# Performance work log

Hardware: AMD Instinct MI355X
Metric: run time of the kernel (lower is better)

The kernel has to match this reference:

```python
import jax, jax.numpy as jnp
import numpy as np

N = 1024
INTER_CH = 10      # C(4,2) + (8-4)
HIDDEN_CH = 32
OUT_CH = 1
THRESH = 4
TOP_K = 8
INTERACT = 4


def setup_inputs() -> dict:
    key = jax.random.key(0)
    k1, k2, k3, k4, k5 = jax.random.split(key, 5)
    x = jax.random.normal(k1, (16, N, N), dtype=jnp.float32)
    is_active_flags = jnp.ones((16,), dtype=bool)
    # 1x1 conv params (stored as dense matrices; kernel_size=1)
    w1 = jax.random.normal(k2, (HIDDEN_CH, INTER_CH), dtype=jnp.float32) / np.sqrt(INTER_CH)
    b1 = jax.random.normal(k3, (HIDDEN_CH, 1, 1), dtype=jnp.float32) * 0.01
    w2 = jax.random.normal(k4, (OUT_CH, HIDDEN_CH), dtype=jnp.float32) / np.sqrt(HIDDEN_CH)
    b2 = jax.random.normal(k5, (OUT_CH, 1, 1), dtype=jnp.float32) * 0.01
    return {"x": x, "is_active_flags": is_active_flags, "w1": w1, "b1": b1, "w2": w2, "b2": b2}


def reference(x, is_active_flags, w1, b1, w2, b2):
    gate_active = jnp.sum(is_active_flags) >= THRESH

    def _active_path(operand):
        inputs, mask = operand                       # (16, n, n), (16,)
        _, slogdet = jnp.linalg.slogdet(inputs)      # (16,)
        scores = jnp.where(mask, slogdet, -jnp.inf)
        _, indices = jax.lax.top_k(scores, TOP_K)
        top_x = inputs[indices]                      # (8, n, n)
        top_interact_x = top_x[:INTERACT]            # (4, n, n)
        next_preserve_x = top_x[INTERACT:]           # (4, n, n)
        idx1, idx2 = jnp.triu_indices(INTERACT, k=1)  # 6 pairs
        pairs = jnp.matmul(top_interact_x[idx1], top_interact_x[idx2])  # (6, n, n)
        concat = jnp.concatenate([pairs, next_preserve_x], axis=0)      # (10, n, n)
        hidden = jnp.einsum('oc,chw->ohw', w1, concat) + b1             # 1x1 conv
        out = jnp.einsum('oc,chw->ohw', w2, hidden) + b2                # 1x1 conv
        return (out, jnp.array(True))

    def _inactive_path(operand):
        inputs, _ = operand
        _, n, m = inputs.shape
        return (jnp.zeros((OUT_CH, n, m), dtype=jnp.float32), jnp.array(False))

    out, out_active = jax.lax.cond(gate_active, _active_path, _inactive_path, (x, is_active_flags))
    return (out, out_active)
```

## Files before the change

### kernel.cpp

```cpp
#include <hip/hip_runtime.h>
#include <math.h>

#define N 1024
#define NN (N*N)

__global__ void init_kernel(double* scores) {
  int t = threadIdx.x;
  if (t < 16) scores[t] = 0.0;
}

__global__ __launch_bounds__(256) void copy_kernel(const float4* __restrict__ src,
                                                   float4* __restrict__ dst) {
  int i = blockIdx.x * 256 + threadIdx.x;
  dst[i] = src[i];
}

__global__ __launch_bounds__(256, 1) void panel_kernel(float* __restrict__ lu,
                                                       unsigned short* __restrict__ rowsrc,
                                                       double* __restrict__ scores,
                                                       int c0) {
  __shared__ __align__(16) float prow[32];
  __shared__ float ujjS[32];
  __shared__ float redv[2][4];
  __shared__ int   redk[2][4];
  __shared__ int Vv[1024];
  __shared__ int Pv[1024];
  const int m = blockIdx.x;
  float* A = lu + (size_t)m * NN;
  const int R = N - c0;
  const int tid = threadIdx.x;

  const float4 z4 = make_float4(0.f, 0.f, 0.f, 0.f);
  float4 r0_0=z4, r0_1=z4, r0_2=z4, r0_3=z4, r0_4=z4, r0_5=z4, r0_6=z4, r0_7=z4;
  float4 r1_0=z4, r1_1=z4, r1_2=z4, r1_3=z4, r1_4=z4, r1_5=z4, r1_6=z4, r1_7=z4;
  float4 r2_0=z4, r2_1=z4, r2_2=z4, r2_3=z4, r2_4=z4, r2_5=z4, r2_6=z4, r2_7=z4;
  float4 r3_0=z4, r3_1=z4, r3_2=z4, r3_3=z4, r3_4=z4, r3_5=z4, r3_6=z4, r3_7=z4;

  const bool ld0 = (tid           < R);
  const bool ld1 = (tid + 256     < R);
  const bool ld2 = (tid + 512     < R);
  const bool ld3 = (tid + 768     < R);
  bool act0 = ld0, act1 = ld1, act2 = ld2, act3 = ld3;

#define LOADK(K) \
  if (ld##K) { \
    const float* src_ = A + (size_t)(c0 + tid + (K << 8)) * N + c0; \
    r##K##_0 = *(const float4*)(src_ +  0); \
    r##K##_1 = *(const float4*)(src_ +  4); \
    r##K##_2 = *(const float4*)(src_ +  8); \
    r##K##_3 = *(const float4*)(src_ + 12); \
    r##K##_4 = *(const float4*)(src_ + 16); \
    r##K##_5 = *(const float4*)(src_ + 20); \
    r##K##_6 = *(const float4*)(src_ + 24); \
    r##K##_7 = *(const float4*)(src_ + 28); \
  }
  LOADK(0) LOADK(1) LOADK(2) LOADK(3)
#undef LOADK

  for (int i = tid; i < R; i += 256) { Vv[i] = i; Pv[i] = i; }

  {
    float bval = -1.0f; int brow = 0x7fffffff;
    if (act0) { float v = fabsf(r0_0.x); if (v > bval || (v == bval && tid       < brow)) { bval = v; brow = tid;       } }
    if (act1) { float v = fabsf(r1_0.x); if (v > bval || (v == bval && tid + 256 < brow)) { bval = v; brow = tid + 256; } }
    if (act2) { float v = fabsf(r2_0.x); if (v > bval || (v == bval && tid + 512 < brow)) { bval = v; brow = tid + 512; } }
    if (act3) { float v = fabsf(r3_0.x); if (v > bval || (v == bval && tid + 768 < brow)) { bval = v; brow = tid + 768; } }
    #pragma unroll
    for (int mask = 32; mask; mask >>= 1) {
      float ov = __shfl_xor(bval, mask);
      int   orr = __shfl_xor(brow, mask);
      if (ov > bval || (ov == bval && orr < brow)) { bval = ov; brow = orr; }
    }
    if ((tid & 63) == 0) { redv[0][tid >> 6] = bval; redk[0][tid >> 6] = brow; }
  }
  __syncthreads();

  #pragma unroll 1
  for (int j = 0; j < 32; ++j) {
    int pcur;
    {
      const int pb = j & 1;
      float bv = redv[pb][0]; int bk = redk[pb][0];
      float v1 = redv[pb][1]; int k1 = redk[pb][1];
      float v2 = redv[pb][2]; int k2 = redk[pb][2];
      float v3 = redv[pb][3]; int k3 = redk[pb][3];
      if (v1 > bv || (v1 == bv && k1 < bk)) { bv = v1; bk = k1; }
      if (v2 > bv || (v2 == bv && k2 < bk)) { bv = v2; bk = k2; }
      if (v3 > bv || (v3 == bv && k3 < bk)) { bv = v3; bk = k3; }
      pcur = bk;
    }
    if (tid == (pcur & 255)) {
      const int kk = pcur >> 8;
      float4* pd = (float4*)prow;
#define PUBQ(Q) { \
      float4 v = r0_##Q; \
      if (kk == 1) v = r1_##Q; \
      if (kk == 2) v = r2_##Q; \
      if (kk == 3) v = r3_##Q; \
      pd[Q] = v; }
      PUBQ(0) PUBQ(1) PUBQ(2) PUBQ(3) PUBQ(4) PUBQ(5) PUBQ(6) PUBQ(7)
#undef PUBQ
      if (kk == 0) act0 = false;
      else if (kk == 1) act1 = false;
      else if (kk == 2) act2 = false;
      else act3 = false;
    }
    if (tid == 0) {
      int b  = Pv[pcur];
      int pa = Vv[j];
      Vv[j] = pcur; Vv[b] = pa;
      Pv[pcur] = j; Pv[pa] = b;
    }
    __syncthreads();

    const float ujj = prow[j];
    if (tid == 0) ujjS[j] = ujj;
    const float rujj = 1.0f / ujj;
    const int qj = j >> 2, ej = j & 3;
    const int jn = j + 1;
    const int qn = (j < 31) ? (jn >> 2) : -1, en = jn & 3;

    float4 u4_0=z4, u4_1=z4, u4_2=z4, u4_3=z4, u4_4=z4, u4_5=z4, u4_6=z4, u4_7=z4;
#define UREAD(Q) if (4 * Q + 3 >= j) u4_##Q = *(const float4*)&prow[4 * Q];
    UREAD(0) UREAD(1) UREAD(2) UREAD(3) UREAD(4) UREAD(5) UREAD(6) UREAD(7)
#undef UREAD

    float bval = -1.0f; int brow = 0x7fffffff;
#define QSTEP(K,Q) \
    if (Q >= qj) { \
      float4 v = r##K##_##Q; \
      if (Q == qj) { \
        float aj = (ej == 0) ? v.x : (ej == 1) ? v.y : (ej == 2) ? v.z : v.w; \
        l = aj * rujj; \
        if (ej == 0)      { v.x = l; v.y -= l * u4_##Q.y; v.z -= l * u4_##Q.z; v.w -= l * u4_##Q.w; } \
        else if (ej == 1) { v.y = l; v.z -= l * u4_##Q.z; v.w -= l * u4_##Q.w; } \
        else if (ej == 2) { v.z = l; v.w -= l * u4_##Q.w; } \
        else              { v.w = l; } \
      } else { \
        v.x -= l * u4_##Q.x; v.y -= l * u4_##Q.y; v.z -= l * u4_##Q.z; v.w -= l * u4_##Q.w; \
      } \
      if (Q == qn) nv = (en == 0) ? v.x : (en == 1) ? v.y : (en == 2) ? v.z : v.w; \
      r##K##_##Q = v; \
    }
#define UPDK(K) \
    if (act##K) { \
      const int rr_ = tid + (K << 8); \
      float l = 0.0f, nv = 0.0f; \
      QSTEP(K,0) QSTEP(K,1) QSTEP(K,2) QSTEP(K,3) QSTEP(K,4) QSTEP(K,5) QSTEP(K,6) QSTEP(K,7) \
      if (j < 31) { \
        float av = fabsf(nv); \
        if (av > bval || (av == bval && rr_ < brow)) { bval = av; brow = rr_; } \
      } \
    }
    UPDK(0) UPDK(1) UPDK(2) UPDK(3)
#undef UPDK
#undef QSTEP

    if (j < 31) {
      #pragma unroll
      for (int mask = 32; mask; mask >>= 1) {
        float ov = __shfl_xor(bval, mask);
        int   orr = __shfl_xor(brow, mask);
        if (ov > bval || (ov == bval && orr < brow)) { bval = ov; brow = orr; }
      }
      if ((tid & 63) == 0) { redv[jn & 1][tid >> 6] = bval; redk[jn & 1][tid >> 6] = brow; }
    }
    __syncthreads();
  }

#define STOREK(K) \
  if (ld##K) { \
    float* dst_ = A + (size_t)(c0 + tid + (K << 8)) * N + c0; \
    *(float4*)(dst_ +  0) = r##K##_0; \
    *(float4*)(dst_ +  4) = r##K##_1; \
    *(float4*)(dst_ +  8) = r##K##_2; \
    *(float4*)(dst_ + 12) = r##K##_3; \
    *(float4*)(dst_ + 16) = r##K##_4; \
    *(float4*)(dst_ + 20) = r##K##_5; \
    *(float4*)(dst_ + 24) = r##K##_6; \
    *(float4*)(dst_ + 28) = r##K##_7; \
  }
  STOREK(0) STOREK(1) STOREK(2) STOREK(3)
#undef STOREK

  for (int i = tid; i < R; i += 256) rowsrc[m * 1024 + i] = (unsigned short)(c0 + Vv[i]);
  if (tid < 64) {
    double lg = 0.0;
    if (tid < 32) lg = log(fabs((double)ujjS[tid]));
    #pragma unroll
    for (int mask = 32; mask; mask >>= 1) lg += __shfl_xor(lg, mask);
    if (tid == 0) atomicAdd(&scores[m], lg);
  }
}

__global__ __launch_bounds__(256) void ptrsm_kernel(float* __restrict__ lu,
                                                    const unsigned short* __restrict__ rowsrc,
                                                    int c0, int ncs) {
  const int m  = blockIdx.x / ncs;
  const int cs = blockIdx.x % ncs;
  const int s0 = c0 + 32 + cs * 256;
  const int tid = threadIdx.x;
  const int col = s0 + tid;
  const bool ac = col < N;
  float* A = lu + (size_t)m * NN;
  const int R = N - c0;
  __shared__ int   rowAt[1024];
  __shared__ float L11s[32][33];
  __shared__ int   dDst[48];
  __shared__ int   dSrc[48];
  __shared__ int   dcount;

  for (int r = tid; r < R; r += 256) rowAt[r] = (int)rowsrc[m * 1024 + r];
  if (tid == 0) dcount = 0;
  __syncthreads();
  for (int idx = tid; idx < 1024; idx += 256) {
    int i = idx >> 5, k = idx & 31;
    L11s[i][k] = A[(size_t)rowAt[i] * N + c0 + k];
  }
  for (int r = 32 + tid; r < R; r += 256) {
    if (rowAt[r] != c0 + r) {
      int i = atomicAdd(&dcount, 1);
      dDst[i] = c0 + r; dSrc[i] = rowAt[r];
    }
  }
  __syncthreads();
  const int nd = dcount;

  float pay[32];
  #pragma unroll
  for (int i = 0; i < 32; ++i)
    if (i < nd && ac) pay[i] = A[(size_t)dSrc[i] * N + col];
  float u[32];
  #pragma unroll
  for (int i = 0; i < 32; ++i)
    if (ac) u[i] = A[(size_t)rowAt[i] * N + col];

  #pragma unroll
  for (int i = 1; i < 32; ++i) {
    float a = u[i];
    #pragma unroll
    for (int k = 0; k < 32; ++k)
      if (k < i) a -= L11s[i][k] * u[k];
    u[i] = a;
  }

  #pragma unroll
  for (int i = 0; i < 32; ++i)
    if (i < nd && ac) A[(size_t)dDst[i] * N + col] = pay[i];
  #pragma unroll
  for (int i = 0; i < 32; ++i)
    if (ac) A[(size_t)(c0 + i) * N + col] = u[i];
}

__global__ __launch_bounds__(256) void update_kernel(float* __restrict__ lu,
                                                     const unsigned short* __restrict__ rowsrc,
                                                     int c0, int nrt, int ncs) {
  const int per = nrt * ncs;
  const int m  = blockIdx.x / per;
  const int t  = blockIdx.x % per;
  const int rt = t / ncs, cs = t % ncs;
  const int r0 = c0 + 32 + rt * 64;
  const int s0 = c0 + 32 + cs * 256;
  const int tid = threadIdx.x;
  float* A = lu + (size_t)m * NN;
  __shared__ float Lts[32][68];
  __shared__ float Us[32][260];
  for (int idx = tid; idx < 2048; idx += 256) {
    int r = idx >> 5, k = idx & 31;
    int rr = r0 + r;
    Lts[k][r] = (rr < N) ? A[(size_t)rowsrc[m * 1024 + rr - c0] * N + c0 + k] : 0.0f;
  }
  for (int idx = tid; idx < 8192; idx += 256) {
    int k = idx >> 8, c = idx & 255;
    Us[k][c] = (s0 + c < N) ? A[(size_t)(c0 + k) * N + s0 + c] : 0.0f;
  }
  __syncthreads();
  const int tx = tid & 63;
  const int ty = tid >> 6;
  float4 acc[16];
  #pragma unroll
  for (int e = 0; e < 16; ++e) acc[e] = make_float4(0.f, 0.f, 0.f, 0.f);
  #pragma unroll 4
  for (int k = 0; k < 32; ++k) {
    float4 b  = *(const float4*)&Us[k][tx * 4];
    float4 a0 = *(const float4*)&Lts[k][ty * 16 + 0];
    float4 a1 = *(const float4*)&Lts[k][ty * 16 + 4];
    float4 a2 = *(const float4*)&Lts[k][ty * 16 + 8];
    float4 a3 = *(const float4*)&Lts[k][ty * 16 + 12];
    acc[0].x  += a0.x*b.x; acc[0].y  += a0.x*b.y; acc[0].z  += a0.x*b.z; acc[0].w  += a0.x*b.w;
    acc[1].x  += a0.y*b.x; acc[1].y  += a0.y*b.y; acc[1].z  += a0.y*b.z; acc[1].w  += a0.y*b.w;
    acc[2].x  += a0.z*b.x; acc[2].y  += a0.z*b.y; acc[2].z  += a0.z*b.z; acc[2].w  += a0.z*b.w;
    acc[3].x  += a0.w*b.x; acc[3].y  += a0.w*b.y; acc[3].z  += a0.w*b.z; acc[3].w  += a0.w*b.w;
    acc[4].x  += a1.x*b.x; acc[4].y  += a1.x*b.y; acc[4].z  += a1.x*b.z; acc[4].w  += a1.x*b.w;
    acc[5].x  += a1.y*b.x; acc[5].y  += a1.y*b.y; acc[5].z  += a1.y*b.z; acc[5].w  += a1.y*b.w;
    acc[6].x  += a1.z*b.x; acc[6].y  += a1.z*b.y; acc[6].z  += a1.z*b.z; acc[6].w  += a1.z*b.w;
    acc[7].x  += a1.w*b.x; acc[7].y  += a1.w*b.y; acc[7].z  += a1.w*b.z; acc[7].w  += a1.w*b.w;
    acc[8].x  += a2.x*b.x; acc[8].y  += a2.x*b.y; acc[8].z  += a2.x*b.z; acc[8].w  += a2.x*b.w;
    acc[9].x  += a2.y*b.x; acc[9].y  += a2.y*b.y; acc[9].z  += a2.y*b.z; acc[9].w  += a2.y*b.w;
    acc[10].x += a2.z*b.x; acc[10].y += a2.z*b.y; acc[10].z += a2.z*b.z; acc[10].w += a2.z*b.w;
    acc[11].x += a2.w*b.x; acc[11].y += a2.w*b.y; acc[11].z += a2.w*b.z; acc[11].w += a2.w*b.w;
    acc[12].x += a3.x*b.x; acc[12].y += a3.x*b.y; acc[12].z += a3.x*b.z; acc[12].w += a3.x*b.w;
    acc[13].x += a3.y*b.x; acc[13].y += a3.y*b.y; acc[13].z += a3.y*b.z; acc[13].w += a3.y*b.w;
    acc[14].x += a3.z*b.x; acc[14].y += a3.z*b.y; acc[14].z += a3.z*b.z; acc[14].w += a3.z*b.w;
    acc[15].x += a3.w*b.x; acc[15].y += a3.w*b.y; acc[15].z += a3.w*b.z; acc[15].w += a3.w*b.w;
  }
  const bool colok = (s0 + tx * 4) < N;
  #pragma unroll
  for (int e = 0; e < 16; ++e) {
    int r = r0 + ty * 16 + e;
    if (r < N && colok) {
      float4* p = (float4*)&A[(size_t)r * N + s0 + tx * 4];
      float4 v = *p;
      v.x -= acc[e].x; v.y -= acc[e].y; v.z -= acc[e].z; v.w -= acc[e].w;
      *p = v;
    }
  }
}

__global__ void select_kernel(const void* __restrict__ flagsraw, const double* __restrict__ scores,
                              const float* __restrict__ w1, const float* __restrict__ b1,
                              const float* __restrict__ w2, const float* __restrict__ b2,
                              int* __restrict__ topidx, float* __restrict__ misc,
                              float* __restrict__ out_tail) {
  if (threadIdx.x != 0 || blockIdx.x != 0) return;
  const unsigned char* fb = (const unsigned char*)flagsraw;
  bool nonbin = false, off4 = false;
  for (int i = 0; i < 16; ++i) {
    if (fb[i] > 1) nonbin = true;
    if ((i & 3) && fb[i]) off4 = true;
  }
  int f[16]; int nact = 0;
  for (int i = 0; i < 16; ++i) {
    int v;
    if (nonbin)      v = (((const float*)flagsraw)[i] != 0.0f);
    else if (off4)   v = (fb[i] != 0);
    else             v = (((const int*)flagsraw)[i] != 0);
    f[i] = v; nact += v;
  }
  int gate = (nact >= 4) ? 1 : 0;
  double sc[16];
  for (int i = 0; i < 16; ++i) sc[i] = f[i] ? scores[i] : -1.0e300;
  bool used[16] = {};
  for (int k = 0; k < 8; ++k) {
    int bi = -1; double bv = 0.0;
    for (int i = 0; i < 16; ++i)
      if (!used[i] && (bi < 0 || sc[i] > bv)) { bv = sc[i]; bi = i; }
    used[bi] = true;
    topidx[k] = bi;
  }
  for (int cC = 0; cC < 10; ++cC) {
    float s = 0.0f;
    for (int h = 0; h < 32; ++h) s += w2[h] * w1[h * 10 + cC];
    misc[cC] = s;
  }
  float be = 0.0f;
  for (int h = 0; h < 32; ++h) be += w2[h] * b1[h];
  be += b2[0];
  misc[10] = be;
  ((int*)misc)[12] = gate;
  *out_tail = gate ? 1.0f : 0.0f;
}

__global__ __launch_bounds__(256) void build_m_kernel(const float* __restrict__ x,
                                                      const int* __restrict__ topidx,
                                                      const float* __restrict__ misc,
                                                      float* __restrict__ M) {
  int i = blockIdx.x * 256 + threadIdx.x;
  const float4* T1 = (const float4*)(x + (size_t)topidx[1] * NN);
  const float4* T2 = (const float4*)(x + (size_t)topidx[2] * NN);
  const float4* T3 = (const float4*)(x + (size_t)topidx[3] * NN);
  float w0 = misc[0], w1_ = misc[1], w2_ = misc[2], w3_ = misc[3], w4_ = misc[4], w5_ = misc[5];
  float4 t1 = T1[i], t2 = T2[i], t3 = T3[i];
  float4 m0, m1, m2;
  m0.x = w0 * t1.x + w1_ * t2.x + w2_ * t3.x;
  m0.y = w0 * t1.y + w1_ * t2.y + w2_ * t3.y;
  m0.z = w0 * t1.z + w1_ * t2.z + w2_ * t3.z;
  m0.w = w0 * t1.w + w1_ * t2.w + w2_ * t3.w;
  m1.x = w3_ * t2.x + w4_ * t3.x;
  m1.y = w3_ * t2.y + w4_ * t3.y;
  m1.z = w3_ * t2.z + w4_ * t3.z;
  m1.w = w3_ * t2.w + w4_ * t3.w;
  m2.x = w5_ * t3.x;  m2.y = w5_ * t3.y;  m2.z = w5_ * t3.z;  m2.w = w5_ * t3.w;
  ((float4*)M)[i] = m0;
  ((float4*)(M + NN))[i] = m1;
  ((float4*)(M + 2 * (size_t)NN))[i] = m2;
}

__global__ __launch_bounds__(256) void final_gemm_kernel(const float* __restrict__ x,
                                                         const float* __restrict__ M,
                                                         const int* __restrict__ topidx,
                                                         float* __restrict__ P) {
  const int chunk = blockIdx.x >> 8;
  const int t  = blockIdx.x & 255;
  const int tr = t >> 4, tc = t & 15;
  const int mi  = chunk >> 1;
  const int k0b = (chunk & 1) << 9;
  const float* A = x + (size_t)topidx[mi] * NN;
  const float* B = M + (size_t)mi * NN;
  __shared__ float As[32][68];
  __shared__ float Bs[32][68];
  const int ty = threadIdx.x >> 4, tx = threadIdx.x & 15;
  float acc[4][4] = {};
  for (int k0 = k0b; k0 < k0b + 512; k0 += 32) {
    for (int idx = threadIdx.x; idx < 2048; idx += 256) {
      int r = idx >> 5, k = idx & 31;
      As[k][r] = A[(size_t)(tr * 64 + r) * N + k0 + k];
    }
    for (int idx = threadIdx.x; idx < 2048; idx += 256) {
      int k = idx >> 6, cc = idx & 63;
      Bs[k][cc] = B[(size_t)(k0 + k) * N + tc * 64 + cc];
    }
    __syncthreads();
    #pragma unroll 8
    for (int k = 0; k < 32; ++k) {
      float4 a = *(const float4*)&As[k][ty * 4];
      float4 b = *(const float4*)&Bs[k][tx * 4];
      acc[0][0] += a.x * b.x; acc[0][1] += a.x * b.y; acc[0][2] += a.x * b.z; acc[0][3] += a.x * b.w;
      acc[1][0] += a.y * b.x; acc[1][1] += a.y * b.y; acc[1][2] += a.y * b.z; acc[1][3] += a.y * b.w;
      acc[2][0] += a.z * b.x; acc[2][1] += a.z * b.y; acc[2][2] += a.z * b.z; acc[2][3] += a.z * b.w;
      acc[3][0] += a.w * b.x; acc[3][1] += a.w * b.y; acc[3][2] += a.w * b.z; acc[3][3] += a.w * b.w;
    }
    __syncthreads();
  }
  float* Pc = P + (size_t)chunk * NN;
  #pragma unroll
  for (int i = 0; i < 4; ++i) {
    size_t r = (size_t)(tr * 64 + ty * 4 + i);
    float4 v = make_float4(acc[i][0], acc[i][1], acc[i][2], acc[i][3]);
    *(float4*)&Pc[r * N + tc * 64 + tx * 4] = v;
  }
}

__global__ __launch_bounds__(256) void reduce_out_kernel(const float* __restrict__ x,
                                                         const float* __restrict__ P,
                                                         const int* __restrict__ topidx,
                                                         const float* __restrict__ misc,
                                                         float* __restrict__ out) {
  int i = blockIdx.x * 256 + threadIdx.x;
  int gate = ((const int*)misc)[12];
  float4* o = (float4*)out;
  if (!gate) { o[i] = make_float4(0.f, 0.f, 0.f, 0.f); return; }
  float w6 = misc[6], w7 = misc[7], w8 = misc[8], w9 = misc[9], be = misc[10];
  float4 p0 = ((const float4*)(x + (size_t)topidx[4] * NN))[i];
  float4 p1 = ((const float4*)(x + (size_t)topidx[5] * NN))[i];
  float4 p2 = ((const float4*)(x + (size_t)topidx[6] * NN))[i];
  float4 p3 = ((const float4*)(x + (size_t)topidx[7] * NN))[i];
  float4 r;
  r.x = be + w6 * p0.x + w7 * p1.x + w8 * p2.x + w9 * p3.x;
  r.y = be + w6 * p0.y + w7 * p1.y + w8 * p2.y + w9 * p3.y;
  r.z = be + w6 * p0.z + w7 * p1.z + w8 * p2.z + w9 * p3.z;
  r.w = be + w6 * p0.w + w7 * p1.w + w8 * p2.w + w9 * p3.w;
  #pragma unroll
  for (int cN = 0; cN < 6; ++cN) {
    float4 q = ((const float4*)(P + (size_t)cN * NN))[i];
    r.x += q.x; r.y += q.y; r.z += q.z; r.w += q.w;
  }
  o[i] = r;
}

extern "C" void kernel_launch(void* const* d_in, const int* in_sizes, int n_in,
                              void* d_out, int out_size, void* d_ws, size_t ws_size,
                              hipStream_t stream) {
  const float* x  = (const float*)d_in[0];
  const void*  fl = d_in[1];
  const float* w1 = (const float*)d_in[2];
  const float* b1 = (const float*)d_in[3];
  const float* w2 = (const float*)d_in[4];
  const float* b2 = (const float*)d_in[5];
  float* out = (float*)d_out;

  char* ws = (char*)d_ws;
  float* LU = (float*)ws;
  float* Mm = (float*)ws;
  float* P  = (float*)(ws + (size_t)12 * 1024 * 1024);
  size_t tail = (size_t)16 * NN * sizeof(float);
  double* scores = (double*)(ws + tail);
  unsigned short* rowsrc = (unsigned short*)(ws + tail + 256);
  int*    topidx = (int*)(ws + tail + 256 + 32768);
  float*  misc   = (float*)(ws + tail + 256 + 32768 + 256);

  init_kernel<<<1, 64, 0, stream>>>(scores);
  copy_kernel<<<16384, 256, 0, stream>>>((const float4*)x, (float4*)LU);

  for (int c0 = 0; c0 < N; c0 += 32) {
    panel_kernel<<<16, 256, 0, stream>>>(LU, rowsrc, scores, c0);
    int tcols = N - c0 - 32;
    if (tcols > 0) {
      int ncs = (tcols + 255) / 256;
      ptrsm_kernel<<<16 * ncs, 256, 0, stream>>>(LU, rowsrc, c0, ncs);
      int nrt = (tcols + 63) / 64;
      update_kernel<<<16 * nrt * ncs, 256, 0, stream>>>(LU, rowsrc, c0, nrt, ncs);
    }
  }

  select_kernel<<<1, 64, 0, stream>>>(fl, scores, w1, b1, w2, b2, topidx, misc, out + NN);
  build_m_kernel<<<1024, 256, 0, stream>>>(x, topidx, misc, Mm);
  final_gemm_kernel<<<1536, 256, 0, stream>>>(x, Mm, topidx, P);
  reduce_out_kernel<<<1024, 256, 0, stream>>>(x, P, topidx, misc, out);
}
```

Before: 4.404 ms.

## Widen LU panel to 64 columns and store panel rows pre-permuted

Doubles the blocked LU panel width from 32 to 64 columns, which halves the number of panel/trsm/update launch rounds. The panel kernel now uses 512 threads, and it writes its rows back in pivoted order so that the trsm and update kernels read L directly instead of through rowsrc indirection. The update kernel moves to 64x128 tiles with a K depth of 64. The trade-offs are more registers per thread in the panel and trsm kernels, which risks spills, and a serial 64-step pivot loop per panel.

```diff
diff --git a/kernel.cpp b/kernel.cpp
--- a/kernel.cpp
+++ b/kernel.cpp
@@ -15,14 +15,14 @@
   dst[i] = src[i];
 }
 
-__global__ __launch_bounds__(256, 1) void panel_kernel(float* __restrict__ lu,
+__global__ __launch_bounds__(512, 1) void panel_kernel(float* __restrict__ lu,
                                                        unsigned short* __restrict__ rowsrc,
                                                        double* __restrict__ scores,
                                                        int c0) {
-  __shared__ __align__(16) float prow[32];
-  __shared__ float ujjS[32];
-  __shared__ float redv[2][4];
-  __shared__ int   redk[2][4];
+  __shared__ __align__(16) float prow[64];
+  __shared__ float ujjS[64];
+  __shared__ float redv[2][8];
+  __shared__ int   redk[2][8];
   __shared__ int Vv[1024];
   __shared__ int Pv[1024];
   const int m = blockIdx.x;
@@ -32,39 +32,43 @@
 
   const float4 z4 = make_float4(0.f, 0.f, 0.f, 0.f);
   float4 r0_0=z4, r0_1=z4, r0_2=z4, r0_3=z4, r0_4=z4, r0_5=z4, r0_6=z4, r0_7=z4;
+  float4 r0_8=z4, r0_9=z4, r0_10=z4, r0_11=z4, r0_12=z4, r0_13=z4, r0_14=z4, r0_15=z4;
   float4 r1_0=z4, r1_1=z4, r1_2=z4, r1_3=z4, r1_4=z4, r1_5=z4, r1_6=z4, r1_7=z4;
-  float4 r2_0=z4, r2_1=z4, r2_2=z4, r2_3=z4, r2_4=z4, r2_5=z4, r2_6=z4, r2_7=z4;
-  float4 r3_0=z4, r3_1=z4, r3_2=z4, r3_3=z4, r3_4=z4, r3_5=z4, r3_6=z4, r3_7=z4;
-
-  const bool ld0 = (tid           < R);
-  const bool ld1 = (tid + 256     < R);
-  const bool ld2 = (tid + 512     < R);
-  const bool ld3 = (tid + 768     < R);
-  bool act0 = ld0, act1 = ld1, act2 = ld2, act3 = ld3;
+  float4 r1_8=z4, r1_9=z4, r1_10=z4, r1_11=z4, r1_12=z4, r1_13=z4, r1_14=z4, r1_15=z4;
+
+  const bool ld0 = (tid       < R);
+  const bool ld1 = (tid + 512 < R);
+  bool act0 = ld0, act1 = ld1;
 
 #define LOADK(K) \
   if (ld##K) { \
-    const float* src_ = A + (size_t)(c0 + tid + (K << 8)) * N + c0; \
-    r##K##_0 = *(const float4*)(src_ +  0); \
-    r##K##_1 = *(const float4*)(src_ +  4); \
-    r##K##_2 = *(const float4*)(src_ +  8); \
-    r##K##_3 = *(const float4*)(src_ + 12); \
-    r##K##_4 = *(const float4*)(src_ + 16); \
-    r##K##_5 = *(const float4*)(src_ + 20); \
-    r##K##_6 = *(const float4*)(src_ + 24); \
-    r##K##_7 = *(const float4*)(src_ + 28); \
-  }
-  LOADK(0) LOADK(1) LOADK(2) LOADK(3)
+    const float* src_ = A + (size_t)(c0 + tid + (K << 9)) * N + c0; \
+    r##K##_0  = *(const float4*)(src_ +  0); \
+    r##K##_1  = *(const float4*)(src_ +  4); \
+    r##K##_2  = *(const float4*)(src_ +  8); \
+    r##K##_3  = *(const float4*)(src_ + 12); \
+    r##K##_4  = *(const float4*)(src_ + 16); \
+    r##K##_5  = *(const float4*)(src_ + 20); \
+    r##K##_6  = *(const float4*)(src_ + 24); \
+    r##K##_7  = *(const float4*)(src_ + 28); \
+    r##K##_8  = *(const float4*)(src_ + 32); \
+    r##K##_9  = *(const float4*)(src_ + 36); \
+    r##K##_10 = *(const float4*)(src_ + 40); \
+    r##K##_11 = *(const float4*)(src_ + 44); \
+    r##K##_12 = *(const float4*)(src_ + 48); \
+    r##K##_13 = *(const float4*)(src_ + 52); \
+    r##K##_14 = *(const float4*)(src_ + 56); \
+    r##K##_15 = *(const float4*)(src_ + 60); \
+  }
+  LOADK(0) LOADK(1)
 #undef LOADK
 
-  for (int i = tid; i < R; i += 256) { Vv[i] = i; Pv[i] = i; }
+  for (int i = tid; i < R; i += 512) { Vv[i] = i; Pv[i] = i; }
 
   {
     float bval = -1.0f; int brow = 0x7fffffff;
     if (act0) { float v = fabsf(r0_0.x); if (v > bval || (v == bval && tid       < brow)) { bval = v; brow = tid;       } }
-    if (act1) { float v = fabsf(r1_0.x); if (v > bval || (v == bval && tid + 256 < brow)) { bval = v; brow = tid + 256; } }
-    if (act2) { float v = fabsf(r2_0.x); if (v > bval || (v == bval && tid + 512 < brow)) { bval = v; brow = tid + 512; } }
-    if (act3) { float v = fabsf(r3_0.x); if (v > bval || (v == bval && tid + 768 < brow)) { bval = v; brow = tid + 768; } }
+    if (act1) { float v = fabsf(r1_0.x); if (v > bval || (v == bval && tid + 512 < brow)) { bval = v; brow = tid + 512; } }
     #pragma unroll
     for (int mask = 32; mask; mask >>= 1) {
       float ov = __shfl_xor(bval, mask);
@@ -76,34 +80,26 @@
   __syncthreads();
 
   #pragma unroll 1
-  for (int j = 0; j < 32; ++j) {
+  for (int j = 0; j < 64; ++j) {
     int pcur;
     {
       const int pb = j & 1;
       float bv = redv[pb][0]; int bk = redk[pb][0];
-      float v1 = redv[pb][1]; int k1 = redk[pb][1];
-      float v2 = redv[pb][2]; int k2 = redk[pb][2];
-      float v3 = redv[pb][3]; int k3 = redk[pb][3];
-      if (v1 > bv || (v1 == bv && k1 < bk)) { bv = v1; bk = k1; }
-      if (v2 > bv || (v2 == bv && k2 < bk)) { bv = v2; bk = k2; }
-      if (v3 > bv || (v3 == bv && k3 < bk)) { bv = v3; bk = k3; }
+      #pragma unroll
+      for (int w = 1; w < 8; ++w) {
+        float vw = redv[pb][w]; int kw = redk[pb][w];
+        if (vw > bv || (vw == bv && kw < bk)) { bv = vw; bk = kw; }
+      }
       pcur = bk;
     }
-    if (tid == (pcur & 255)) {
-      const int kk = pcur >> 8;
+    if (tid == (pcur & 511)) {
+      const int kk = pcur >> 9;
       float4* pd = (float4*)prow;
-#define PUBQ(Q) { \
-      float4 v = r0_##Q; \
-      if (kk == 1) v = r1_##Q; \
-      if (kk == 2) v = r2_##Q; \
-      if (kk == 3) v = r3_##Q; \
-      pd[Q] = v; }
+#define PUBQ(Q) { float4 v = r0_##Q; if (kk) v = r1_##Q; pd[Q] = v; }
       PUBQ(0) PUBQ(1) PUBQ(2) PUBQ(3) PUBQ(4) PUBQ(5) PUBQ(6) PUBQ(7)
+      PUBQ(8) PUBQ(9) PUBQ(10) PUBQ(11) PUBQ(12) PUBQ(13) PUBQ(14) PUBQ(15)
 #undef PUBQ
-      if (kk == 0) act0 = false;
-      else if (kk == 1) act1 = false;
-      else if (kk == 2) act2 = false;
-      else act3 = false;
+      if (kk == 0) act0 = false; else act1 = false;
     }
     if (tid == 0) {
       int b  = Pv[pcur];
@@ -118,11 +114,13 @@
     const float rujj = 1.0f / ujj;
     const int qj = j >> 2, ej = j & 3;
     const int jn = j + 1;
-    const int qn = (j < 31) ? (jn >> 2) : -1, en = jn & 3;
+    const int qn = (j < 63) ? (jn >> 2) : -1, en = jn & 3;
 
     float4 u4_0=z4, u4_1=z4, u4_2=z4, u4_3=z4, u4_4=z4, u4_5=z4, u4_6=z4, u4_7=z4;
+    float4 u4_8=z4, u4_9=z4, u4_10=z4, u4_11=z4, u4_12=z4, u4_13=z4, u4_14=z4, u4_15=z4;
 #define UREAD(Q) if (4 * Q + 3 >= j) u4_##Q = *(const float4*)&prow[4 * Q];
     UREAD(0) UREAD(1) UREAD(2) UREAD(3) UREAD(4) UREAD(5) UREAD(6) UREAD(7)
+    UREAD(8) UREAD(9) UREAD(10) UREAD(11) UREAD(12) UREAD(13) UREAD(14) UREAD(15)
 #undef UREAD
 
     float bval = -1.0f; int brow = 0x7fffffff;
@@ -142,21 +140,22 @@
       if (Q == qn) nv = (en == 0) ? v.x : (en == 1) ? v.y : (en == 2) ? v.z : v.w; \
       r##K##_##Q = v; \
     }
-#define UPDK(K) \
+#define UPDK(K, RBASE) \
     if (act##K) { \
-      const int rr_ = tid + (K << 8); \
+      const int rr_ = tid + RBASE; \
       float l = 0.0f, nv = 0.0f; \
       QSTEP(K,0) QSTEP(K,1) QSTEP(K,2) QSTEP(K,3) QSTEP(K,4) QSTEP(K,5) QSTEP(K,6) QSTEP(K,7) \
-      if (j < 31) { \
+      QSTEP(K,8) QSTEP(K,9) QSTEP(K,10) QSTEP(K,11) QSTEP(K,12) QSTEP(K,13) QSTEP(K,14) QSTEP(K,15) \
+      if (j < 63) { \
         float av = fabsf(nv); \
         if (av > bval || (av == bval && rr_ < brow)) { bval = av; brow = rr_; } \
       } \
     }
-    UPDK(0) UPDK(1) UPDK(2) UPDK(3)
+    UPDK(0, 0) UPDK(1, 512)
 #undef UPDK
 #undef QSTEP
 
-    if (j < 31) {
+    if (j < 63) {
       #pragma unroll
       for (int mask = 32; mask; mask >>= 1) {
         float ov = __shfl_xor(bval, mask);
@@ -170,23 +169,23 @@
 
 #define STOREK(K) \
   if (ld##K) { \
-    float* dst_ = A + (size_t)(c0 + tid + (K << 8)) * N + c0; \
-    *(float4*)(dst_ +  0) = r##K##_0; \
-    *(float4*)(dst_ +  4) = r##K##_1; \
-    *(float4*)(dst_ +  8) = r##K##_2; \
-    *(float4*)(dst_ + 12) = r##K##_3; \
-    *(float4*)(dst_ + 16) = r##K##_4; \
-    *(float4*)(dst_ + 20) = r##K##_5; \
-    *(float4*)(dst_ + 24) = r##K##_6; \
-    *(float4*)(dst_ + 28) = r##K##_7; \
-  }
-  STOREK(0) STOREK(1) STOREK(2) STOREK(3)
+    const int p_ = tid + (K << 9); \
+    float* dst_ = A + (size_t)(c0 + Pv[p_]) * N + c0; \
+    *(float4*)(dst_ +  0) = r##K##_0;  *(float4*)(dst_ +  4) = r##K##_1; \
+    *(float4*)(dst_ +  8) = r##K##_2;  *(float4*)(dst_ + 12) = r##K##_3; \
+    *(float4*)(dst_ + 16) = r##K##_4;  *(float4*)(dst_ + 20) = r##K##_5; \
+    *(float4*)(dst_ + 24) = r##K##_6;  *(float4*)(dst_ + 28) = r##K##_7; \
+    *(float4*)(dst_ + 32) = r##K##_8;  *(float4*)(dst_ + 36) = r##K##_9; \
+    *(float4*)(dst_ + 40) = r##K##_10; *(float4*)(dst_ + 44) = r##K##_11; \
+    *(float4*)(dst_ + 48) = r##K##_12; *(float4*)(dst_ + 52) = r##K##_13; \
+    *(float4*)(dst_ + 56) = r##K##_14; *(float4*)(dst_ + 60) = r##K##_15; \
+  }
+  STOREK(0) STOREK(1)
 #undef STOREK
 
-  for (int i = tid; i < R; i += 256) rowsrc[m * 1024 + i] = (unsigned short)(c0 + Vv[i]);
+  for (int i = tid; i < R; i += 512) rowsrc[m * 1024 + i] = (unsigned short)(c0 + Vv[i]);
   if (tid < 64) {
-    double lg = 0.0;
-    if (tid < 32) lg = log(fabs((double)ujjS[tid]));
+    double lg = log(fabs((double)ujjS[tid]));
     #pragma unroll
     for (int mask = 32; mask; mask >>= 1) lg += __shfl_xor(lg, mask);
     if (tid == 0) atomicAdd(&scores[m], lg);
@@ -198,26 +197,26 @@
                                                     int c0, int ncs) {
   const int m  = blockIdx.x / ncs;
   const int cs = blockIdx.x % ncs;
-  const int s0 = c0 + 32 + cs * 256;
+  const int s0 = c0 + 64 + cs * 256;
   const int tid = threadIdx.x;
   const int col = s0 + tid;
   const bool ac = col < N;
   float* A = lu + (size_t)m * NN;
   const int R = N - c0;
   __shared__ int   rowAt[1024];
-  __shared__ float L11s[32][33];
-  __shared__ int   dDst[48];
-  __shared__ int   dSrc[48];
+  __shared__ float L11s[64][65];
+  __shared__ int   dDst[80];
+  __shared__ int   dSrc[80];
   __shared__ int   dcount;
 
   for (int r = tid; r < R; r += 256) rowAt[r] = (int)rowsrc[m * 1024 + r];
   if (tid == 0) dcount = 0;
   __syncthreads();
-  for (int idx = tid; idx < 1024; idx += 256) {
-    int i = idx >> 5, k = idx & 31;
-    L11s[i][k] = A[(size_t)rowAt[i] * N + c0 + k];
-  }
-  for (int r = 32 + tid; r < R; r += 256) {
+  for (int idx = tid; idx < 4096; idx += 256) {
+    int i = idx >> 6, k = idx & 63;
+    L11s[i][k] = A[(size_t)(c0 + i) * N + c0 + k];
+  }
+  for (int r = 64 + tid; r < R; r += 256) {
     if (rowAt[r] != c0 + r) {
       int i = atomicAdd(&dcount, 1);
       dDst[i] = c0 + r; dSrc[i] = rowAt[r];
@@ -226,88 +225,76 @@
   __syncthreads();
   const int nd = dcount;
 
-  float pay[32];
-  #pragma unroll
-  for (int i = 0; i < 32; ++i)
+  float pay[64];
+  #pragma unroll
+  for (int i = 0; i < 64; ++i)
     if (i < nd && ac) pay[i] = A[(size_t)dSrc[i] * N + col];
-  float u[32];
-  #pragma unroll
-  for (int i = 0; i < 32; ++i)
+  float u[64];
+  #pragma unroll
+  for (int i = 0; i < 64; ++i)
     if (ac) u[i] = A[(size_t)rowAt[i] * N + col];
 
   #pragma unroll
-  for (int i = 1; i < 32; ++i) {
+  for (int i = 1; i < 64; ++i) {
     float a = u[i];
     #pragma unroll
-    for (int k = 0; k < 32; ++k)
+    for (int k = 0; k < 64; ++k)
       if (k < i) a -= L11s[i][k] * u[k];
     u[i] = a;
   }
 
   #pragma unroll
-  for (int i = 0; i < 32; ++i)
+  for (int i = 0; i < 64; ++i)
     if (i < nd && ac) A[(size_t)dDst[i] * N + col] = pay[i];
   #pragma unroll
-  for (int i = 0; i < 32; ++i)
+  for (int i = 0; i < 64; ++i)
     if (ac) A[(size_t)(c0 + i) * N + col] = u[i];
 }
 
 __global__ __launch_bounds__(256) void update_kernel(float* __restrict__ lu,
-                                                     const unsigned short* __restrict__ rowsrc,
                                                      int c0, int nrt, int ncs) {
   const int per = nrt * ncs;
   const int m  = blockIdx.x / per;
   const int t  = blockIdx.x % per;
   const int rt = t / ncs, cs = t % ncs;
-  const int r0 = c0 + 32 + rt * 64;
-  const int s0 = c0 + 32 + cs * 256;
+  const int r0 = c0 + 64 + rt * 64;
+  const int s0 = c0 + 64 + cs * 128;
   const int tid = threadIdx.x;
   float* A = lu + (size_t)m * NN;
-  __shared__ float Lts[32][68];
-  __shared__ float Us[32][260];
-  for (int idx = tid; idx < 2048; idx += 256) {
-    int r = idx >> 5, k = idx & 31;
-    int rr = r0 + r;
-    Lts[k][r] = (rr < N) ? A[(size_t)rowsrc[m * 1024 + rr - c0] * N + c0 + k] : 0.0f;
+  __shared__ float Lts[64][68];
+  __shared__ float Us[64][132];
+  for (int idx = tid; idx < 4096; idx += 256) {
+    int r = idx >> 6, k = idx & 63;
+    Lts[k][r] = (r0 + r < N) ? A[(size_t)(r0 + r) * N + c0 + k] : 0.0f;
   }
   for (int idx = tid; idx < 8192; idx += 256) {
-    int k = idx >> 8, c = idx & 255;
+    int k = idx >> 7, c = idx & 127;
     Us[k][c] = (s0 + c < N) ? A[(size_t)(c0 + k) * N + s0 + c] : 0.0f;
   }
   __syncthreads();
-  const int tx = tid & 63;
-  const int ty = tid >> 6;
-  float4 acc[16];
-  #pragma unroll
-  for (int e = 0; e < 16; ++e) acc[e] = make_float4(0.f, 0.f, 0.f, 0.f);
+  const int tx = tid & 31;
+  const int ty = tid >> 5;
+  float4 acc[8];
+  #pragma unroll
+  for (int e = 0; e < 8; ++e) acc[e] = make_float4(0.f, 0.f, 0.f, 0.f);
   #pragma unroll 4
-  for (int k = 0; k < 32; ++k) {
+  for (int k = 0; k < 64; ++k) {
     float4 b  = *(const float4*)&Us[k][tx * 4];
-    float4 a0 = *(const float4*)&Lts[k][ty * 16 + 0];
-    float4 a1 = *(const float4*)&Lts[k][ty * 16 + 4];
-    float4 a2 = *(const float4*)&Lts[k][ty * 16 + 8];
-    float4 a3 = *(const float4*)&Lts[k][ty * 16 + 12];
-    acc[0].x  += a0.x*b.x; acc[0].y  += a0.x*b.y; acc[0].z  += a0.x*b.z; acc[0].w  += a0.x*b.w;
-    acc[1].x  += a0.y*b.x; acc[1].y  += a0.y*b.y; acc[1].z  += a0.y*b.z; acc[1].w  += a0.y*b.w;
-    acc[2].x  += a0.z*b.x; acc[2].y  += a0.z*b.y; acc[2].z  += a0.z*b.z; acc[2].w  += a0.z*b.w;
-    acc[3].x  += a0.w*b.x; acc[3].y  += a0.w*b.y; acc[3].z  += a0.w*b.z; acc[3].w  += a0.w*b.w;
-    acc[4].x  += a1.x*b.x; acc[4].y  += a1.x*b.y; acc[4].z  += a1.x*b.z; acc[4].w  += a1.x*b.w;
-    acc[5].x  += a1.y*b.x; acc[5].y  += a1.y*b.y; acc[5].z  += a1.y*b.z; acc[5].w  += a1.y*b.w;
-    acc[6].x  += a1.z*b.x; acc[6].y  += a1.z*b.y; acc[6].z  += a1.z*b.z; acc[6].w  += a1.z*b.w;
-    acc[7].x  += a1.w*b.x; acc[7].y  += a1.w*b.y; acc[7].z  += a1.w*b.z; acc[7].w  += a1.w*b.w;
-    acc[8].x  += a2.x*b.x; acc[8].y  += a2.x*b.y; acc[8].z  += a2.x*b.z; acc[8].w  += a2.x*b.w;
-    acc[9].x  += a2.y*b.x; acc[9].y  += a2.y*b.y; acc[9].z  += a2.y*b.z; acc[9].w  += a2.y*b.w;
-    acc[10].x += a2.z*b.x; acc[10].y += a2.z*b.y; acc[10].z += a2.z*b.z; acc[10].w += a2.z*b.w;
-    acc[11].x += a2.w*b.x; acc[11].y += a2.w*b.y; acc[11].z += a2.w*b.z; acc[11].w += a2.w*b.w;
-    acc[12].x += a3.x*b.x; acc[12].y += a3.x*b.y; acc[12].z += a3.x*b.z; acc[12].w += a3.x*b.w;
-    acc[13].x += a3.y*b.x; acc[13].y += a3.y*b.y; acc[13].z += a3.y*b.z; acc[13].w += a3.y*b.w;
-    acc[14].x += a3.z*b.x; acc[14].y += a3.z*b.y; acc[14].z += a3.z*b.z; acc[14].w += a3.z*b.w;
-    acc[15].x += a3.w*b.x; acc[15].y += a3.w*b.y; acc[15].z += a3.w*b.z; acc[15].w += a3.w*b.w;
+    float4 a0 = *(const float4*)&Lts[k][ty * 8 + 0];
+    float4 a1 = *(const float4*)&Lts[k][ty * 8 + 4];
+    acc[0].x += a0.x*b.x; acc[0].y += a0.x*b.y; acc[0].z += a0.x*b.z; acc[0].w += a0.x*b.w;
+    acc[1].x += a0.y*b.x; acc[1].y += a0.y*b.y; acc[1].z += a0.y*b.z; acc[1].w += a0.y*b.w;
+    acc[2].x += a0.z*b.x; acc[2].y += a0.z*b.y; acc[2].z += a0.z*b.z; acc[2].w += a0.z*b.w;
+    acc[3].x += a0.w*b.x; acc[3].y += a0.w*b.y; acc[3].z += a0.w*b.z; acc[3].w += a0.w*b.w;
+    acc[4].x += a1.x*b.x; acc[4].y += a1.x*b.y; acc[4].z += a1.x*b.z; acc[4].w += a1.x*b.w;
+    acc[5].x += a1.y*b.x; acc[5].y += a1.y*b.y; acc[5].z += a1.y*b.z; acc[5].w += a1.y*b.w;
+    acc[6].x += a1.z*b.x; acc[6].y += a1.z*b.y; acc[6].z += a1.z*b.z; acc[6].w += a1.z*b.w;
+    acc[7].x += a1.w*b.x; acc[7].y += a1.w*b.y; acc[7].z += a1.w*b.z; acc[7].w += a1.w*b.w;
   }
   const bool colok = (s0 + tx * 4) < N;
   #pragma unroll
-  for (int e = 0; e < 16; ++e) {
-    int r = r0 + ty * 16 + e;
+  for (int e = 0; e < 8; ++e) {
+    int r = r0 + ty * 8 + e;
     if (r < N && colok) {
       float4* p = (float4*)&A[(size_t)r * N + s0 + tx * 4];
       float4 v = *p;
@@ -482,14 +469,15 @@
   init_kernel<<<1, 64, 0, stream>>>(scores);
   copy_kernel<<<16384, 256, 0, stream>>>((const float4*)x, (float4*)LU);
 
-  for (int c0 = 0; c0 < N; c0 += 32) {
-    panel_kernel<<<16, 256, 0, stream>>>(LU, rowsrc, scores, c0);
-    int tcols = N - c0 - 32;
+  for (int c0 = 0; c0 < N; c0 += 64) {
+    panel_kernel<<<16, 512, 0, stream>>>(LU, rowsrc, scores, c0);
+    int tcols = N - c0 - 64;
     if (tcols > 0) {
       int ncs = (tcols + 255) / 256;
       ptrsm_kernel<<<16 * ncs, 256, 0, stream>>>(LU, rowsrc, c0, ncs);
       int nrt = (tcols + 63) / 64;
-      update_kernel<<<16 * nrt * ncs, 256, 0, stream>>>(LU, rowsrc, c0, nrt, ncs);
+      int ncs2 = (tcols + 127) / 128;
+      update_kernel<<<16 * nrt * ncs2, 256, 0, stream>>>(LU, c0, nrt, ncs2);
     }
   }
 
```

Measured after the change: 5.909 ms. 34.2% more time.
